# Kernel optimization log

Hardware: AMD Instinct MI355X
Metric: run time of the kernel (lower is better)

Reference implementation:

```python
import jax, jax.numpy as jnp
import numpy as np

V, H, B, S, L = 32000, 1024, 128, 256, 2


def setup_inputs() -> dict:
    key = jax.random.key(0)
    ks = jax.random.split(key, 20)
    p = lambda k, shape: (0.02 * jax.random.normal(k, shape)).astype(jnp.float32)
    return {
        "input_ids": jax.random.randint(ks[0], (B,), 0, V),
        "hidden": jax.random.normal(ks[1], (L, B, H), dtype=jnp.float32),
        "encoder_outputs": jax.random.normal(ks[2], (S, B, H), dtype=jnp.float32),
        "embed_table": p(ks[3], (V, H)),
        "W_attn": p(ks[4], (H, 2 * H)),
        "b_attn": p(ks[5], (H,)),
        "v": p(ks[6], (H,)),
        "w_ih0": p(ks[7], (3 * H, H)), "w_hh0": p(ks[8], (3 * H, H)),
        "b_ih0": p(ks[9], (3 * H,)), "b_hh0": p(ks[10], (3 * H,)),
        "w_ih1": p(ks[11], (3 * H, H)), "w_hh1": p(ks[12], (3 * H, H)),
        "b_ih1": p(ks[13], (3 * H,)), "b_hh1": p(ks[14], (3 * H,)),
        "W_concat": p(ks[15], (H, 2 * H)), "b_concat": p(ks[16], (H,)),
        "W_out": p(ks[17], (V, H)), "b_out": p(ks[18], (V,)),
    }


def gru_cell(x, h, w_ih, w_hh, b_ih, b_hh):
    # PyTorch GRU cell: gates order (r, z, n)
    gi = x @ w_ih.T + b_ih  # [B, 3H]
    gh = h @ w_hh.T + b_hh
    ir, iz, inn = jnp.split(gi, 3, axis=-1)
    hr, hz, hn = jnp.split(gh, 3, axis=-1)
    r = jax.nn.sigmoid(ir + hr)
    z = jax.nn.sigmoid(iz + hz)
    n = jnp.tanh(inn + r * hn)
    return (1.0 - z) * n + z * h


def reference(input_ids, hidden, encoder_outputs, embed_table, W_attn, b_attn, v,
              w_ih0, w_hh0, b_ih0, b_hh0, w_ih1, w_hh1, b_ih1, b_hh1,
              W_concat, b_concat, W_out, b_out):
    # embedding lookup (dropout is identity in eval mode)
    x = embed_table[input_ids]  # [B, H]
    # 2-layer GRU, single time step
    h0 = gru_cell(x, hidden[0], w_ih0, w_hh0, b_ih0, b_hh0)
    h1 = gru_cell(h0, hidden[1], w_ih1, w_hh1, b_ih1, b_hh1)
    rnn_out = h1                                   # [B, H]
    new_hidden = jnp.stack([h0, h1], axis=0)       # [L, B, H]
    # Bahdanau-style scorer: energy = Linear(cat(h, enc)); score = v . energy
    h_b = jnp.broadcast_to(rnn_out[None, :, :], encoder_outputs.shape)  # [S, B, H]
    feats = jnp.concatenate([h_b, encoder_outputs], axis=-1)            # [S, B, 2H]
    energy = jnp.einsum('sbe,he->sbh', feats, W_attn) + b_attn          # [S, B, H]
    scores = jnp.einsum('sbh,h->bs', energy, v)                         # [B, S]
    attn_weights = jax.nn.softmax(scores, axis=1)                       # [B, S]
    # context = attn_weights @ encoder_outputs (bmm)
    context = jnp.einsum('bs,sbh->bh', attn_weights, encoder_outputs)   # [B, H]
    concat_in = jnp.concatenate([rnn_out, context], axis=-1)            # [B, 2H]
    concat_out = jnp.tanh(concat_in @ W_concat.T + b_concat)            # [B, H]
    output = concat_out @ W_out.T + b_out                               # [B, V]
    return (output, new_hidden, attn_weights[:, None, :])
```

## Files before the change

### kernel.cpp

```cpp
#include <hip/hip_runtime.h>
#include <cstdint>
#include <cstddef>

typedef __attribute__((ext_vector_type(4))) float f32x4;
typedef __attribute__((ext_vector_type(8))) __bf16 bf16x8;
typedef __attribute__((ext_vector_type(8))) short short8;

__device__ __forceinline__ unsigned short f2bf(float f) {
  unsigned u = __builtin_bit_cast(unsigned, f);
  u += 0x7FFFu + ((u >> 16) & 1u);
  return (unsigned short)(u >> 16);
}
__device__ __forceinline__ unsigned pack2(float a, float b) {
  return (unsigned)f2bf(a) | ((unsigned)f2bf(b) << 16);
}

__device__ __forceinline__ void async16(const void* g, void* l) {
  __builtin_amdgcn_global_load_lds((const __attribute__((address_space(1))) unsigned int*)g,
                                   (__attribute__((address_space(3))) unsigned int*)l, 16, 0, 0);
}

struct GemmArgs {
  const unsigned short* A;
  const float* W;
  const float* bias;
  float* C;
};

template <int BN, int WAVES_M, int WAVES_N>
__global__ __launch_bounds__(256, 4) void gemm_bt(GemmArgs g0, GemmArgs g1, int lda, int ldw,
                                                  int N, int Kseg, int seg_stride) {
  constexpr int WM = 128 / WAVES_M, WN = BN / WAVES_N;
  constexpr int MT = WM / 16, NT = WN / 16;
  __shared__ unsigned short a_lds[2][128 * 64];
  __shared__ unsigned short w_lds[2][BN * 64];

  const GemmArgs g = (blockIdx.y == 0) ? g0 : g1;
  const int kbase = blockIdx.z * Kseg;
  const int tid = threadIdx.x;
  const int wave = tid >> 6, lane = tid & 63;
  const int quad = lane >> 4, l16 = lane & 15;
  const int n0 = blockIdx.x * BN;
  const int wm = (wave / WAVES_N) * WM, wn = (wave % WAVES_N) * WN;
  const int niter = Kseg >> 6;

  f32x4 wv[2];

  auto stageA = [&](int k0, int buf) {
#pragma unroll
    for (int i = 0; i < 4; ++i) {
      int chunk = (wave * 4 + i) * 64 + lane;
      int r = chunk >> 3;
      int c = (chunk & 7) ^ (r & 7);
      async16(g.A + (size_t)r * lda + (k0 + c * 8), &a_lds[buf][chunk * 8]);
    }
  };
  auto loadW = [&](int k0) {
    if constexpr (BN == 32) {
      const float* p = g.W + (size_t)(n0 + (tid >> 3)) * ldw + k0 + (tid & 7) * 8;
      wv[0] = *(const f32x4*)p;
      wv[1] = *(const f32x4*)(p + 4);
    } else {
      const float* p = g.W + (size_t)(n0 + (tid >> 4)) * ldw + k0 + ((tid >> 1) & 7) * 8 + (tid & 1) * 4;
      wv[0] = *(const f32x4*)p;
    }
  };
  auto writeW = [&](int buf) {
    if constexpr (BN == 32) {
      int wr = tid >> 3, wc = tid & 7;
      uint4 pk{pack2(wv[0].x, wv[0].y), pack2(wv[0].z, wv[0].w),
               pack2(wv[1].x, wv[1].y), pack2(wv[1].z, wv[1].w)};
      *(uint4*)&w_lds[buf][(wr * 8 + (wc ^ (wr & 7))) * 8] = pk;
    } else {
      int wr = tid >> 4, wc = (tid >> 1) & 7, half = tid & 1;
      uint2 pk{pack2(wv[0].x, wv[0].y), pack2(wv[0].z, wv[0].w)};
      *(uint2*)&w_lds[buf][(wr * 8 + (wc ^ (wr & 7))) * 8 + half * 4] = pk;
    }
  };

  f32x4 acc[MT][NT] = {};

  stageA(kbase, 0);
  loadW(kbase);
  writeW(0);
  __syncthreads();

  for (int ki = 0; ki < niter; ++ki) {
    const int cur = ki & 1;
    const bool more = (ki + 1 < niter);
    if (more) {
      stageA(kbase + (ki + 1) * 64, cur ^ 1);
      loadW(kbase + (ki + 1) * 64);
    }
#pragma unroll
    for (int kh = 0; kh < 2; ++kh) {
      const int c = kh * 4 + quad;
      bf16x8 af[MT], wf[NT];
#pragma unroll
      for (int mt = 0; mt < MT; ++mt) {
        int m = wm + mt * 16 + l16;
        af[mt] = __builtin_bit_cast(bf16x8, *(const short8*)&a_lds[cur][(m * 8 + (c ^ (m & 7))) * 8]);
      }
#pragma unroll
      for (int nt = 0; nt < NT; ++nt) {
        int n = wn + nt * 16 + l16;
        wf[nt] = __builtin_bit_cast(bf16x8, *(const short8*)&w_lds[cur][(n * 8 + (c ^ (n & 7))) * 8]);
      }
#pragma unroll
      for (int mt = 0; mt < MT; ++mt)
#pragma unroll
        for (int nt = 0; nt < NT; ++nt)
          acc[mt][nt] = __builtin_amdgcn_mfma_f32_16x16x32_bf16(af[mt], wf[nt], acc[mt][nt], 0, 0, 0);
    }
    if (more) writeW(cur ^ 1);
    __syncthreads();
  }

  float* C = g.C + (size_t)blockIdx.z * seg_stride;
#pragma unroll
  for (int mt = 0; mt < MT; ++mt)
#pragma unroll
    for (int nt = 0; nt < NT; ++nt) {
      int n = n0 + wn + nt * 16 + l16;
      float bv = (blockIdx.z == 0) ? g.bias[n] : 0.f;
#pragma unroll
      for (int r = 0; r < 4; ++r) {
        int m = wm + mt * 16 + quad * 4 + r;
        C[(size_t)m * N + n] = acc[mt][nt][r] + bv;
      }
    }
}

__global__ __launch_bounds__(256) void prep_kernel(const int* __restrict__ ids,
                                                   const float* __restrict__ hidden,
                                                   const float* __restrict__ embed,
                                                   unsigned short* A0, unsigned short* Hh0,
                                                   unsigned short* Hh1) {
  int job = blockIdx.x >> 7, m = blockIdx.x & 127, t = threadIdx.x;
  const float* src;
  unsigned short* dst;
  if (job == 0) { src = embed + (size_t)ids[m] * 1024; dst = A0; }
  else if (job == 1) { src = hidden + (size_t)m * 1024; dst = Hh0; }
  else { src = hidden + 131072 + (size_t)m * 1024; dst = Hh1; }
  f32x4 v = ((const f32x4*)src)[t];
  uint2 pk{pack2(v.x, v.y), pack2(v.z, v.w)};
  *(uint2*)(dst + (size_t)m * 1024 + t * 4) = pk;
}

__global__ __launch_bounds__(256) void u2_kernel(const float* __restrict__ W_attn,
                                                 const float* __restrict__ v,
                                                 float* __restrict__ u2) {
  int eb = blockIdx.x & 3, hc = blockIdx.x >> 2;
  int e = eb * 256 + threadIdx.x;
  float acc = 0.f;
  int h0 = hc * 32;
#pragma unroll 4
  for (int h = h0; h < h0 + 32; ++h) acc += v[h] * W_attn[(size_t)h * 2048 + 1024 + e];
  atomicAdd(u2 + e, acc);
}

__global__ __launch_bounds__(256) void scores_kernel(const float* __restrict__ enc,
                                                     const float* __restrict__ u2,
                                                     float* __restrict__ sct) {
  int wave = threadIdx.x >> 6, lane = threadIdx.x & 63;
  const f32x4* u4 = (const f32x4*)u2;
  f32x4 uv[4];
#pragma unroll
  for (int p = 0; p < 4; ++p) uv[p] = u4[p * 64 + lane];
  int row0 = (blockIdx.x * 4 + wave) * 4;
  const f32x4* base = (const f32x4*)enc;
  f32x4 ev[4][4];
#pragma unroll
  for (int r = 0; r < 4; ++r)
#pragma unroll
    for (int p = 0; p < 4; ++p) ev[r][p] = base[(size_t)(row0 + r) * 256 + p * 64 + lane];
  float a[4];
#pragma unroll
  for (int r = 0; r < 4; ++r) {
    float s = 0.f;
#pragma unroll
    for (int p = 0; p < 4; ++p)
      s += ev[r][p].x * uv[p].x + ev[r][p].y * uv[p].y + ev[r][p].z * uv[p].z + ev[r][p].w * uv[p].w;
    a[r] = s;
  }
#pragma unroll
  for (int r = 0; r < 4; ++r)
#pragma unroll
    for (int off = 32; off > 0; off >>= 1) a[r] += __shfl_down(a[r], off, 64);
  if (lane == 0) {
#pragma unroll
    for (int r = 0; r < 4; ++r) {
      int row = row0 + r;
      sct[(row & 127) * 256 + (row >> 7)] = a[r];
    }
  }
}

__global__ __launch_bounds__(256) void softmax_kernel(const float* __restrict__ sct,
                                                      float* __restrict__ attn) {
  __shared__ float wmax[4], wsum[4];
  int b = blockIdx.x, t = threadIdx.x;
  int wave = t >> 6, lane = t & 63;
  float sc = sct[b * 256 + t];
  float m = sc;
#pragma unroll
  for (int off = 32; off > 0; off >>= 1) m = fmaxf(m, __shfl_xor(m, off, 64));
  if (lane == 0) wmax[wave] = m;
  __syncthreads();
  float m4 = fmaxf(fmaxf(wmax[0], wmax[1]), fmaxf(wmax[2], wmax[3]));
  float e = __expf(sc - m4);
  float s = e;
#pragma unroll
  for (int off = 32; off > 0; off >>= 1) s += __shfl_xor(s, off, 64);
  if (lane == 0) wsum[wave] = s;
  __syncthreads();
  float tot = (wsum[0] + wsum[1]) + (wsum[2] + wsum[3]);
  attn[b * 256 + t] = e / tot;
}

__global__ __launch_bounds__(256) void context_kernel(const float* __restrict__ enc,
                                                      const float* __restrict__ attn,
                                                      unsigned short* __restrict__ catin) {
  __shared__ float sm[256];
  int b = blockIdx.x >> 2, hc = blockIdx.x & 3;
  int t = threadIdx.x;
  sm[t] = attn[b * 256 + t];
  __syncthreads();
  int h = hc * 256 + t;
  const float* ep = enc + (size_t)b * 1024 + h;
  float a[16];
#pragma unroll
  for (int i = 0; i < 16; ++i) a[i] = 0.f;
  for (int s0 = 0; s0 < 256; s0 += 16)
#pragma unroll
    for (int i = 0; i < 16; ++i) a[i] += sm[s0 + i] * ep[(size_t)(s0 + i) * 131072];
  float tot = 0.f;
#pragma unroll
  for (int i = 0; i < 16; ++i) tot += a[i];
  catin[(size_t)b * 2048 + 1024 + h] = f2bf(tot);
}

__global__ __launch_bounds__(256) void gru_gate(const float* __restrict__ gi,
                                                const float* __restrict__ gh,
                                                const float* __restrict__ h_prev,
                                                float* __restrict__ h_out,
                                                unsigned short* __restrict__ h_bf, int bf_ld) {
  constexpr int SEG = 393216;
  int b = blockIdx.x, j = threadIdx.x * 4;
  const float* gib = gi + (size_t)b * 3072;
  const float* ghb = gh + (size_t)b * 3072;
  f32x4 ir = *(const f32x4*)(gib + j) + *(const f32x4*)(gib + SEG + j);
  f32x4 iz = *(const f32x4*)(gib + 1024 + j) + *(const f32x4*)(gib + SEG + 1024 + j);
  f32x4 in_ = *(const f32x4*)(gib + 2048 + j) + *(const f32x4*)(gib + SEG + 2048 + j);
  f32x4 hr = *(const f32x4*)(ghb + j) + *(const f32x4*)(ghb + SEG + j);
  f32x4 hz = *(const f32x4*)(ghb + 1024 + j) + *(const f32x4*)(ghb + SEG + 1024 + j);
  f32x4 hn = *(const f32x4*)(ghb + 2048 + j) + *(const f32x4*)(ghb + SEG + 2048 + j);
  f32x4 hp = *(const f32x4*)(h_prev + (size_t)b * 1024 + j);
  f32x4 ho;
#pragma unroll
  for (int c = 0; c < 4; ++c) {
    float r = 1.f / (1.f + __expf(-(ir[c] + hr[c])));
    float z = 1.f / (1.f + __expf(-(iz[c] + hz[c])));
    float n = tanhf(in_[c] + r * hn[c]);
    ho[c] = (1.f - z) * n + z * hp[c];
  }
  *(f32x4*)(h_out + (size_t)b * 1024 + j) = ho;
  uint2 pk{pack2(ho.x, ho.y), pack2(ho.z, ho.w)};
  *(uint2*)(h_bf + (size_t)b * bf_ld + j) = pk;
}

__global__ __launch_bounds__(256) void cat_fix(const float* __restrict__ part,
                                               unsigned short* __restrict__ catbf) {
  int m = blockIdx.x, j = threadIdx.x * 4;
  const float* p = part + (size_t)m * 1024 + j;
  f32x4 s = *(const f32x4*)p + *(const f32x4*)(p + 131072) + *(const f32x4*)(p + 262144) +
            *(const f32x4*)(p + 393216);
  f32x4 o;
#pragma unroll
  for (int c = 0; c < 4; ++c) o[c] = tanhf(s[c]);
  uint2 pk{pack2(o.x, o.y), pack2(o.z, o.w)};
  *(uint2*)(catbf + (size_t)m * 1024 + j) = pk;
}

extern "C" void kernel_launch(void* const* d_in, const int* in_sizes, int n_in,
                              void* d_out_, int out_size, void* d_ws, size_t ws_size,
                              hipStream_t stream) {
  const int* ids = (const int*)d_in[0];
  const float* hidden = (const float*)d_in[1];
  const float* enc = (const float*)d_in[2];
  const float* embed = (const float*)d_in[3];
  const float* W_attn = (const float*)d_in[4];
  const float* v = (const float*)d_in[6];
  const float* w_ih0 = (const float*)d_in[7];
  const float* w_hh0 = (const float*)d_in[8];
  const float* b_ih0 = (const float*)d_in[9];
  const float* b_hh0 = (const float*)d_in[10];
  const float* w_ih1 = (const float*)d_in[11];
  const float* w_hh1 = (const float*)d_in[12];
  const float* b_ih1 = (const float*)d_in[13];
  const float* b_hh1 = (const float*)d_in[14];
  const float* W_cat = (const float*)d_in[15];
  const float* b_cat = (const float*)d_in[16];
  const float* W_out = (const float*)d_in[17];
  const float* b_out = (const float*)d_in[18];

  float* out = (float*)d_out_;
  float* h0 = out + 4096000;
  float* h1 = out + 4227072;
  float* attn = out + 4358144;

  float* ws = (float*)d_ws;
  float* gi = ws;
  float* gh = ws + 786432;
  float* u2 = ws + 1572864;
  float* sct = ws + 1573888;
  float* catp = ws + 1606656;
  unsigned short* bfb = (unsigned short*)(ws + 2130944);
  unsigned short* A0 = bfb;
  unsigned short* Hh0 = bfb + 131072;
  unsigned short* Hh1 = bfb + 262144;
  unsigned short* h0bf = bfb + 393216;
  unsigned short* catin = bfb + 524288;
  unsigned short* catbf = bfb + 786432;

  hipMemsetAsync(u2, 0, 1024 * sizeof(float), stream);
  prep_kernel<<<384, 256, 0, stream>>>(ids, hidden, embed, A0, Hh0, Hh1);
  u2_kernel<<<128, 256, 0, stream>>>(W_attn, v, u2);
  scores_kernel<<<2048, 256, 0, stream>>>(enc, u2, sct);
  softmax_kernel<<<128, 256, 0, stream>>>(sct, attn);
  context_kernel<<<512, 256, 0, stream>>>(enc, attn, catin);

  {
    GemmArgs ai{A0, w_ih0, b_ih0, gi}, ah{Hh0, w_hh0, b_hh0, gh};
    gemm_bt<16, 4, 1><<<dim3(192, 2, 2), 256, 0, stream>>>(ai, ah, 1024, 1024, 3072, 512, 393216);
  }
  gru_gate<<<128, 256, 0, stream>>>(gi, gh, hidden, h0, h0bf, 1024);

  {
    GemmArgs ai{h0bf, w_ih1, b_ih1, gi}, ah{Hh1, w_hh1, b_hh1, gh};
    gemm_bt<16, 4, 1><<<dim3(192, 2, 2), 256, 0, stream>>>(ai, ah, 1024, 1024, 3072, 512, 393216);
  }
  gru_gate<<<128, 256, 0, stream>>>(gi, gh, hidden + 131072, h1, catin, 2048);

  {
    GemmArgs ac{catin, W_cat, b_cat, catp};
    gemm_bt<16, 4, 1><<<dim3(64, 1, 4), 256, 0, stream>>>(ac, ac, 2048, 2048, 1024, 512, 131072);
  }
  cat_fix<<<128, 256, 0, stream>>>(catp, catbf);

  {
    GemmArgs ao{catbf, W_out, b_out, out};
    gemm_bt<32, 2, 2><<<dim3(1000, 1, 1), 256, 0, stream>>>(ao, ao, 1024, 1024, 32000, 1024, 0);
  }
}
```

Baseline: 472.0 us.

## Merge independent attention and GRU stages into combined launches, deepen weight prefetch

Kernels that do not depend on each other now share launches. The memset, prep and u2 work become one kernel (u2 is reduced in LDS instead of with atomics). Attention scores run alongside the first GRU GEMM, and the fused softmax+context runs alongside the first gate kernel. Separately, the GEMM body now prefetches fp32 weight tiles two k-steps ahead in registers, which raises register pressure. The aim is to cut launch count and idle gaps between small kernels, at the cost of more heterogeneous blocks within one grid.

```diff
diff --git a/kernel.cpp b/kernel.cpp
--- a/kernel.cpp
+++ b/kernel.cpp
@@ -14,10 +14,12 @@
 __device__ __forceinline__ unsigned pack2(float a, float b) {
   return (unsigned)f2bf(a) | ((unsigned)f2bf(b) << 16);
 }
-
 __device__ __forceinline__ void async16(const void* g, void* l) {
   __builtin_amdgcn_global_load_lds((const __attribute__((address_space(1))) unsigned int*)g,
                                    (__attribute__((address_space(3))) unsigned int*)l, 16, 0, 0);
+}
+__device__ __forceinline__ bf16x8 ldsFrag(const unsigned short* p) {
+  return __builtin_bit_cast(bf16x8, *(const short8*)p);
 }
 
 struct GemmArgs {
@@ -28,23 +30,24 @@
 };
 
 template <int BN, int WAVES_M, int WAVES_N>
-__global__ __launch_bounds__(256, 4) void gemm_bt(GemmArgs g0, GemmArgs g1, int lda, int ldw,
-                                                  int N, int Kseg, int seg_stride) {
+__device__ __forceinline__ void gemm_body(const unsigned short* __restrict__ A,
+                                          const float* __restrict__ W,
+                                          const float* __restrict__ bias,
+                                          float* __restrict__ Cout, int lda, int ldw, int N,
+                                          int Kseg, int kbase, int nblk, bool addbias,
+                                          unsigned short* a_lds, unsigned short* w_lds) {
   constexpr int WM = 128 / WAVES_M, WN = BN / WAVES_N;
   constexpr int MT = WM / 16, NT = WN / 16;
-  __shared__ unsigned short a_lds[2][128 * 64];
-  __shared__ unsigned short w_lds[2][BN * 64];
-
-  const GemmArgs g = (blockIdx.y == 0) ? g0 : g1;
-  const int kbase = blockIdx.z * Kseg;
+  constexpr int WCH = (BN == 32) ? 2 : 1;
+
   const int tid = threadIdx.x;
   const int wave = tid >> 6, lane = tid & 63;
   const int quad = lane >> 4, l16 = lane & 15;
-  const int n0 = blockIdx.x * BN;
+  const int n0 = nblk * BN;
   const int wm = (wave / WAVES_N) * WM, wn = (wave % WAVES_N) * WN;
   const int niter = Kseg >> 6;
 
-  f32x4 wv[2];
+  f32x4 wv[2][WCH];
 
   auto stageA = [&](int k0, int buf) {
 #pragma unroll
@@ -52,59 +55,60 @@
       int chunk = (wave * 4 + i) * 64 + lane;
       int r = chunk >> 3;
       int c = (chunk & 7) ^ (r & 7);
-      async16(g.A + (size_t)r * lda + (k0 + c * 8), &a_lds[buf][chunk * 8]);
+      async16(A + (size_t)r * lda + k0 + c * 8, a_lds + (size_t)buf * 8192 + chunk * 8);
     }
   };
-  auto loadW = [&](int k0) {
+  auto loadW = [&](int k0, int set) {
     if constexpr (BN == 32) {
-      const float* p = g.W + (size_t)(n0 + (tid >> 3)) * ldw + k0 + (tid & 7) * 8;
-      wv[0] = *(const f32x4*)p;
-      wv[1] = *(const f32x4*)(p + 4);
+      const float* p = W + (size_t)(n0 + (tid >> 3)) * ldw + k0 + (tid & 7) * 8;
+      wv[set][0] = *(const f32x4*)p;
+      wv[set][1] = *(const f32x4*)(p + 4);
     } else {
-      const float* p = g.W + (size_t)(n0 + (tid >> 4)) * ldw + k0 + ((tid >> 1) & 7) * 8 + (tid & 1) * 4;
-      wv[0] = *(const f32x4*)p;
+      const float* p = W + (size_t)(n0 + (tid >> 4)) * ldw + k0 + ((tid >> 1) & 7) * 8 + (tid & 1) * 4;
+      wv[set][0] = *(const f32x4*)p;
     }
   };
-  auto writeW = [&](int buf) {
+  auto writeW = [&](int set, int buf) {
+    unsigned short* wb = w_lds + (size_t)buf * BN * 64;
     if constexpr (BN == 32) {
       int wr = tid >> 3, wc = tid & 7;
-      uint4 pk{pack2(wv[0].x, wv[0].y), pack2(wv[0].z, wv[0].w),
-               pack2(wv[1].x, wv[1].y), pack2(wv[1].z, wv[1].w)};
-      *(uint4*)&w_lds[buf][(wr * 8 + (wc ^ (wr & 7))) * 8] = pk;
+      uint4 pk{pack2(wv[set][0].x, wv[set][0].y), pack2(wv[set][0].z, wv[set][0].w),
+               pack2(wv[set][1].x, wv[set][1].y), pack2(wv[set][1].z, wv[set][1].w)};
+      *(uint4*)&wb[(wr * 8 + (wc ^ (wr & 7))) * 8] = pk;
     } else {
       int wr = tid >> 4, wc = (tid >> 1) & 7, half = tid & 1;
-      uint2 pk{pack2(wv[0].x, wv[0].y), pack2(wv[0].z, wv[0].w)};
-      *(uint2*)&w_lds[buf][(wr * 8 + (wc ^ (wr & 7))) * 8 + half * 4] = pk;
+      uint2 pk{pack2(wv[set][0].x, wv[set][0].y), pack2(wv[set][0].z, wv[set][0].w)};
+      *(uint2*)&wb[(wr * 8 + (wc ^ (wr & 7))) * 8 + half * 4] = pk;
     }
   };
 
   f32x4 acc[MT][NT] = {};
 
+  loadW(kbase, 0);
   stageA(kbase, 0);
-  loadW(kbase);
-  writeW(0);
+  loadW(kbase + 64, 1);
+  writeW(0, 0);
   __syncthreads();
 
   for (int ki = 0; ki < niter; ++ki) {
     const int cur = ki & 1;
-    const bool more = (ki + 1 < niter);
-    if (more) {
-      stageA(kbase + (ki + 1) * 64, cur ^ 1);
-      loadW(kbase + (ki + 1) * 64);
-    }
+    if (ki + 1 < niter) stageA(kbase + (ki + 1) * 64, cur ^ 1);
+    if (ki + 2 < niter) loadW(kbase + (ki + 2) * 64, cur);
 #pragma unroll
     for (int kh = 0; kh < 2; ++kh) {
       const int c = kh * 4 + quad;
+      const unsigned short* ab = a_lds + (size_t)cur * 8192;
+      const unsigned short* wb = w_lds + (size_t)cur * BN * 64;
       bf16x8 af[MT], wf[NT];
 #pragma unroll
       for (int mt = 0; mt < MT; ++mt) {
         int m = wm + mt * 16 + l16;
-        af[mt] = __builtin_bit_cast(bf16x8, *(const short8*)&a_lds[cur][(m * 8 + (c ^ (m & 7))) * 8]);
+        af[mt] = ldsFrag(&ab[(m * 8 + (c ^ (m & 7))) * 8]);
       }
 #pragma unroll
       for (int nt = 0; nt < NT; ++nt) {
         int n = wn + nt * 16 + l16;
-        wf[nt] = __builtin_bit_cast(bf16x8, *(const short8*)&w_lds[cur][(n * 8 + (c ^ (n & 7))) * 8]);
+        wf[nt] = ldsFrag(&wb[(n * 8 + (c ^ (n & 7))) * 8]);
       }
 #pragma unroll
       for (int mt = 0; mt < MT; ++mt)
@@ -112,62 +116,44 @@
         for (int nt = 0; nt < NT; ++nt)
           acc[mt][nt] = __builtin_amdgcn_mfma_f32_16x16x32_bf16(af[mt], wf[nt], acc[mt][nt], 0, 0, 0);
     }
-    if (more) writeW(cur ^ 1);
+    if (ki + 1 < niter) writeW(cur ^ 1, cur ^ 1);
     __syncthreads();
   }
 
-  float* C = g.C + (size_t)blockIdx.z * seg_stride;
 #pragma unroll
   for (int mt = 0; mt < MT; ++mt)
 #pragma unroll
     for (int nt = 0; nt < NT; ++nt) {
       int n = n0 + wn + nt * 16 + l16;
-      float bv = (blockIdx.z == 0) ? g.bias[n] : 0.f;
+      float bv = addbias ? bias[n] : 0.f;
 #pragma unroll
       for (int r = 0; r < 4; ++r) {
         int m = wm + mt * 16 + quad * 4 + r;
-        C[(size_t)m * N + n] = acc[mt][nt][r] + bv;
+        Cout[(size_t)m * N + n] = acc[mt][nt][r] + bv;
       }
     }
 }
 
-__global__ __launch_bounds__(256) void prep_kernel(const int* __restrict__ ids,
-                                                   const float* __restrict__ hidden,
-                                                   const float* __restrict__ embed,
-                                                   unsigned short* A0, unsigned short* Hh0,
-                                                   unsigned short* Hh1) {
-  int job = blockIdx.x >> 7, m = blockIdx.x & 127, t = threadIdx.x;
-  const float* src;
-  unsigned short* dst;
-  if (job == 0) { src = embed + (size_t)ids[m] * 1024; dst = A0; }
-  else if (job == 1) { src = hidden + (size_t)m * 1024; dst = Hh0; }
-  else { src = hidden + 131072 + (size_t)m * 1024; dst = Hh1; }
-  f32x4 v = ((const f32x4*)src)[t];
-  uint2 pk{pack2(v.x, v.y), pack2(v.z, v.w)};
-  *(uint2*)(dst + (size_t)m * 1024 + t * 4) = pk;
-}
-
-__global__ __launch_bounds__(256) void u2_kernel(const float* __restrict__ W_attn,
-                                                 const float* __restrict__ v,
-                                                 float* __restrict__ u2) {
-  int eb = blockIdx.x & 3, hc = blockIdx.x >> 2;
-  int e = eb * 256 + threadIdx.x;
-  float acc = 0.f;
-  int h0 = hc * 32;
-#pragma unroll 4
-  for (int h = h0; h < h0 + 32; ++h) acc += v[h] * W_attn[(size_t)h * 2048 + 1024 + e];
-  atomicAdd(u2 + e, acc);
-}
-
-__global__ __launch_bounds__(256) void scores_kernel(const float* __restrict__ enc,
-                                                     const float* __restrict__ u2,
-                                                     float* __restrict__ sct) {
+template <int BN, int WAVES_M, int WAVES_N>
+__global__ __launch_bounds__(256, 4) void gemm_k(GemmArgs g0, GemmArgs g1, int lda, int ldw,
+                                                 int N, int Kseg, int seg_stride) {
+  __shared__ unsigned short a_lds[2 * 128 * 64];
+  __shared__ unsigned short w_lds[2 * BN * 64];
+  const GemmArgs g = (blockIdx.y == 0) ? g0 : g1;
+  const int kseg = blockIdx.z;
+  gemm_body<BN, WAVES_M, WAVES_N>(g.A, g.W, g.bias, g.C + (size_t)kseg * seg_stride, lda, ldw,
+                                  N, Kseg, kseg * Kseg, blockIdx.x, kseg == 0, a_lds, w_lds);
+}
+
+__device__ __forceinline__ void scores_body(int bx, const float* __restrict__ enc,
+                                            const float* __restrict__ u2,
+                                            float* __restrict__ sct) {
   int wave = threadIdx.x >> 6, lane = threadIdx.x & 63;
   const f32x4* u4 = (const f32x4*)u2;
   f32x4 uv[4];
 #pragma unroll
   for (int p = 0; p < 4; ++p) uv[p] = u4[p * 64 + lane];
-  int row0 = (blockIdx.x * 4 + wave) * 4;
+  int row0 = (bx * 4 + wave) * 4;
   const f32x4* base = (const f32x4*)enc;
   f32x4 ev[4][4];
 #pragma unroll
@@ -196,36 +182,54 @@
   }
 }
 
-__global__ __launch_bounds__(256) void softmax_kernel(const float* __restrict__ sct,
-                                                      float* __restrict__ attn) {
-  __shared__ float wmax[4], wsum[4];
-  int b = blockIdx.x, t = threadIdx.x;
-  int wave = t >> 6, lane = t & 63;
+__global__ __launch_bounds__(256, 4) void mega_sg(const float* __restrict__ enc,
+                                                  const float* __restrict__ u2,
+                                                  float* __restrict__ sct, GemmArgs g0,
+                                                  GemmArgs g1, int lda, int ldw, int N, int Kseg,
+                                                  int seg_stride) {
+  __shared__ unsigned short a_lds[2 * 128 * 64];
+  __shared__ unsigned short w_lds[2 * 16 * 64];
+  int bx = blockIdx.x;
+  if (bx < 2048) {
+    scores_body(bx, enc, u2, sct);
+    return;
+  }
+  int idx = bx - 2048;
+  int nt = idx % 192;
+  int pair = (idx / 192) & 1;
+  int kseg = idx / 384;
+  const GemmArgs g = pair ? g1 : g0;
+  gemm_body<16, 4, 1>(g.A, g.W, g.bias, g.C + (size_t)kseg * seg_stride, lda, ldw, N, Kseg,
+                      kseg * Kseg, nt, kseg == 0, a_lds, w_lds);
+}
+
+__device__ __forceinline__ void ctx_body(int bx, const float* __restrict__ enc,
+                                         const float* __restrict__ sct, float* __restrict__ attn,
+                                         unsigned short* __restrict__ catin) {
+  __shared__ float sm[256];
+  __shared__ float wred[8];
+  int b = bx >> 2, hc = bx & 3, t = threadIdx.x;
+  int wv_ = t >> 6, l = t & 63;
+
   float sc = sct[b * 256 + t];
-  float m = sc;
-#pragma unroll
-  for (int off = 32; off > 0; off >>= 1) m = fmaxf(m, __shfl_xor(m, off, 64));
-  if (lane == 0) wmax[wave] = m;
+  float mx = sc;
+#pragma unroll
+  for (int off = 32; off > 0; off >>= 1) mx = fmaxf(mx, __shfl_xor(mx, off, 64));
+  if (l == 0) wred[wv_] = mx;
   __syncthreads();
-  float m4 = fmaxf(fmaxf(wmax[0], wmax[1]), fmaxf(wmax[2], wmax[3]));
+  float m4 = fmaxf(fmaxf(wred[0], wred[1]), fmaxf(wred[2], wred[3]));
   float e = __expf(sc - m4);
   float s = e;
 #pragma unroll
   for (int off = 32; off > 0; off >>= 1) s += __shfl_xor(s, off, 64);
-  if (lane == 0) wsum[wave] = s;
+  if (l == 0) wred[4 + wv_] = s;
   __syncthreads();
-  float tot = (wsum[0] + wsum[1]) + (wsum[2] + wsum[3]);
-  attn[b * 256 + t] = e / tot;
-}
-
-__global__ __launch_bounds__(256) void context_kernel(const float* __restrict__ enc,
-                                                      const float* __restrict__ attn,
-                                                      unsigned short* __restrict__ catin) {
-  __shared__ float sm[256];
-  int b = blockIdx.x >> 2, hc = blockIdx.x & 3;
-  int t = threadIdx.x;
-  sm[t] = attn[b * 256 + t];
+  float tot = (wred[4] + wred[5]) + (wred[6] + wred[7]);
+  float aw = e / tot;
+  sm[t] = aw;
+  if (hc == 0) attn[b * 256 + t] = aw;
   __syncthreads();
+
   int h = hc * 256 + t;
   const float* ep = enc + (size_t)b * 1024 + h;
   float a[16];
@@ -234,19 +238,19 @@
   for (int s0 = 0; s0 < 256; s0 += 16)
 #pragma unroll
     for (int i = 0; i < 16; ++i) a[i] += sm[s0 + i] * ep[(size_t)(s0 + i) * 131072];
-  float tot = 0.f;
-#pragma unroll
-  for (int i = 0; i < 16; ++i) tot += a[i];
-  catin[(size_t)b * 2048 + 1024 + h] = f2bf(tot);
-}
-
-__global__ __launch_bounds__(256) void gru_gate(const float* __restrict__ gi,
-                                                const float* __restrict__ gh,
-                                                const float* __restrict__ h_prev,
-                                                float* __restrict__ h_out,
-                                                unsigned short* __restrict__ h_bf, int bf_ld) {
+  float ctx = 0.f;
+#pragma unroll
+  for (int i = 0; i < 16; ++i) ctx += a[i];
+  catin[(size_t)b * 2048 + 1024 + h] = f2bf(ctx);
+}
+
+__device__ __forceinline__ void gate_body(int b, const float* __restrict__ gi,
+                                          const float* __restrict__ gh,
+                                          const float* __restrict__ h_prev,
+                                          float* __restrict__ h_out,
+                                          unsigned short* __restrict__ h_bf, int bf_ld) {
   constexpr int SEG = 393216;
-  int b = blockIdx.x, j = threadIdx.x * 4;
+  int j = threadIdx.x * 4;
   const float* gib = gi + (size_t)b * 3072;
   const float* ghb = gh + (size_t)b * 3072;
   f32x4 ir = *(const f32x4*)(gib + j) + *(const f32x4*)(gib + SEG + j);
@@ -267,6 +271,62 @@
   *(f32x4*)(h_out + (size_t)b * 1024 + j) = ho;
   uint2 pk{pack2(ho.x, ho.y), pack2(ho.z, ho.w)};
   *(uint2*)(h_bf + (size_t)b * bf_ld + j) = pk;
+}
+
+__global__ __launch_bounds__(256) void mega_cg(const float* __restrict__ enc,
+                                               const float* __restrict__ sct,
+                                               float* __restrict__ attn,
+                                               unsigned short* __restrict__ catin,
+                                               const float* __restrict__ gi,
+                                               const float* __restrict__ gh,
+                                               const float* __restrict__ h_prev,
+                                               float* __restrict__ h_out,
+                                               unsigned short* __restrict__ h_bf, int bf_ld) {
+  int bx = blockIdx.x;
+  if (bx < 512) ctx_body(bx, enc, sct, attn, catin);
+  else gate_body(bx - 512, gi, gh, h_prev, h_out, h_bf, bf_ld);
+}
+
+__global__ __launch_bounds__(256) void gate_k(const float* __restrict__ gi,
+                                              const float* __restrict__ gh,
+                                              const float* __restrict__ h_prev,
+                                              float* __restrict__ h_out,
+                                              unsigned short* __restrict__ h_bf, int bf_ld) {
+  gate_body(blockIdx.x, gi, gh, h_prev, h_out, h_bf, bf_ld);
+}
+
+__global__ __launch_bounds__(256) void prep_u2(const int* __restrict__ ids,
+                                               const float* __restrict__ hidden,
+                                               const float* __restrict__ embed,
+                                               const float* __restrict__ W_attn,
+                                               const float* __restrict__ v,
+                                               unsigned short* A0, unsigned short* Hh0,
+                                               unsigned short* Hh1, float* __restrict__ u2) {
+  int blk = blockIdx.x, t = threadIdx.x;
+  if (blk < 384) {
+    int job = blk >> 7, m = blk & 127;
+    const float* src;
+    unsigned short* dst;
+    if (job == 0) { src = embed + (size_t)ids[m] * 1024; dst = A0; }
+    else if (job == 1) { src = hidden + (size_t)m * 1024; dst = Hh0; }
+    else { src = hidden + 131072 + (size_t)m * 1024; dst = Hh1; }
+    f32x4 val = ((const f32x4*)src)[t];
+    uint2 pk{pack2(val.x, val.y), pack2(val.z, val.w)};
+    *(uint2*)(dst + (size_t)m * 1024 + t * 4) = pk;
+  } else {
+    __shared__ float red[4][64];
+    int lb = blk - 384;
+    int wv_ = t >> 6, l = t & 63;
+    int e = lb * 64 + l;
+    const float* col = W_attn + 1024 + e;
+    float acc = 0.f;
+    int h0 = wv_ * 256;
+#pragma unroll 8
+    for (int h = h0; h < h0 + 256; ++h) acc += v[h] * col[(size_t)h * 2048];
+    red[wv_][l] = acc;
+    __syncthreads();
+    if (t < 64) u2[lb * 64 + t] = red[0][t] + red[1][t] + red[2][t] + red[3][t];
+  }
 }
 
 __global__ __launch_bounds__(256) void cat_fix(const float* __restrict__ part,
@@ -323,33 +383,31 @@
   unsigned short* catin = bfb + 524288;
   unsigned short* catbf = bfb + 786432;
 
-  hipMemsetAsync(u2, 0, 1024 * sizeof(float), stream);
-  prep_kernel<<<384, 256, 0, stream>>>(ids, hidden, embed, A0, Hh0, Hh1);
-  u2_kernel<<<128, 256, 0, stream>>>(W_attn, v, u2);
-  scores_kernel<<<2048, 256, 0, stream>>>(enc, u2, sct);
-  softmax_kernel<<<128, 256, 0, stream>>>(sct, attn);
-  context_kernel<<<512, 256, 0, stream>>>(enc, attn, catin);
+  prep_u2<<<400, 256, 0, stream>>>(ids, hidden, embed, W_attn, v, A0, Hh0, Hh1, u2);
 
   {
     GemmArgs ai{A0, w_ih0, b_ih0, gi}, ah{Hh0, w_hh0, b_hh0, gh};
-    gemm_bt<16, 4, 1><<<dim3(192, 2, 2), 256, 0, stream>>>(ai, ah, 1024, 1024, 3072, 512, 393216);
-  }
-  gru_gate<<<128, 256, 0, stream>>>(gi, gh, hidden, h0, h0bf, 1024);
+    mega_sg<<<2816, 256, 0, stream>>>(enc, u2, sct, ai, ah, 1024, 1024, 3072, 512, 393216);
+  }
+
+  mega_cg<<<640, 256, 0, stream>>>(enc, sct, attn, catin, gi, gh, hidden, h0, h0bf, 1024);
 
   {
     GemmArgs ai{h0bf, w_ih1, b_ih1, gi}, ah{Hh1, w_hh1, b_hh1, gh};
-    gemm_bt<16, 4, 1><<<dim3(192, 2, 2), 256, 0, stream>>>(ai, ah, 1024, 1024, 3072, 512, 393216);
-  }
-  gru_gate<<<128, 256, 0, stream>>>(gi, gh, hidden + 131072, h1, catin, 2048);
+    gemm_k<16, 4, 1><<<dim3(192, 2, 2), 256, 0, stream>>>(ai, ah, 1024, 1024, 3072, 512, 393216);
+  }
+
+  gate_k<<<128, 256, 0, stream>>>(gi, gh, hidden + 131072, h1, catin, 2048);
 
   {
-    GemmArgs ac{catin, W_cat, b_cat, catp};
-    gemm_bt<16, 4, 1><<<dim3(64, 1, 4), 256, 0, stream>>>(ac, ac, 2048, 2048, 1024, 512, 131072);
-  }
+    GemmArgs ac{catin, W_cat, b_cat, catp}, dummy = ac;
+    gemm_k<16, 4, 1><<<dim3(64, 1, 4), 256, 0, stream>>>(ac, dummy, 2048, 2048, 1024, 512, 131072);
+  }
+
   cat_fix<<<128, 256, 0, stream>>>(catp, catbf);
 
   {
-    GemmArgs ao{catbf, W_out, b_out, out};
-    gemm_bt<32, 2, 2><<<dim3(1000, 1, 1), 256, 0, stream>>>(ao, ao, 1024, 1024, 32000, 1024, 0);
-  }
-}
+    GemmArgs ao{catbf, W_out, b_out, out}, dummy = ao;
+    gemm_k<32, 2, 2><<<dim3(1000, 1, 1), 256, 0, stream>>>(ao, dummy, 1024, 1024, 32000, 1024, 0);
+  }
+}
```

Measured after the change: 494.6 us. 4.8% more time.
